# Optimization experiments

Measured on AMD Instinct MI355X. Metric: run time of the kernel, lower is better.

Reference implementation:

```python
import jax, jax.numpy as jnp
import numpy as np

N = 20000
E = 320000
DIM_IN, DIM_H, DIM_OUT, HEADS = 500, 32, 16, 8
NEG_SLOPE = 0.2


def _glorot(key, shape, fan_in, fan_out):
    s = jnp.sqrt(6.0 / (fan_in + fan_out))
    return jax.random.uniform(key, shape, jnp.float32, -s, s)


def setup_inputs() -> dict:
    key = jax.random.key(0)
    ks = jax.random.split(key, 16)
    x = jax.random.normal(ks[0], (N, DIM_IN), jnp.float32)
    edge_index = jax.random.randint(ks[1], (2, E), 0, N, jnp.int64)
    h1 = HEADS * DIM_H   # 256
    h2 = HEADS * DIM_OUT  # 128
    return {
        "x": x,
        "edge_index": edge_index,
        # layer 1: GATv2Conv(500, 32, heads=8), concat -> 256
        "W1l": _glorot(ks[2], (h1, DIM_IN), DIM_IN, h1),
        "b1l": jnp.zeros((h1,), jnp.float32),
        "W1r": _glorot(ks[3], (h1, DIM_IN), DIM_IN, h1),
        "b1r": jnp.zeros((h1,), jnp.float32),
        "att1": _glorot(ks[4], (HEADS, DIM_H), DIM_H, 1),
        "bias1": jnp.zeros((h1,), jnp.float32),
        # layer 2: GATv2Conv(256, 16, heads=8), concat -> 128
        "W2l": _glorot(ks[5], (h2, h1), h1, h2),
        "b2l": jnp.zeros((h2,), jnp.float32),
        "W2r": _glorot(ks[6], (h2, h1), h1, h2),
        "b2r": jnp.zeros((h2,), jnp.float32),
        "att2": _glorot(ks[7], (HEADS, DIM_OUT), DIM_OUT, 1),
        "bias2": jnp.zeros((h2,), jnp.float32),
    }


def _gatv2_layer(x, Wl, bl, Wr, br, att, bias, src, dst, heads, out_ch):
    n = x.shape[0]
    xl = (x @ Wl.T + bl).reshape(n, heads, out_ch)  # source transform
    xr = (x @ Wr.T + br).reshape(n, heads, out_ch)  # target transform
    e = xl[src] + xr[dst]                            # [E', H, C]
    e = jnp.where(e >= 0, e, NEG_SLOPE * e)          # LeakyReLU(0.2)
    logits = jnp.einsum('ehc,hc->eh', e, att)        # [E', H]
    # segment softmax over incoming edges of each dst node
    m = jax.ops.segment_max(logits, dst, num_segments=n)
    ex = jnp.exp(logits - m[dst])
    denom = jax.ops.segment_sum(ex, dst, num_segments=n)
    alpha = ex / denom[dst]                          # [E', H]
    out = jax.ops.segment_sum(xl[src] * alpha[:, :, None], dst, num_segments=n)
    return out.reshape(n, heads * out_ch) + bias


def reference(x, edge_index, W1l, b1l, W1r, b1r, att1, bias1,
              W2l, b2l, W2r, b2r, att2, bias2):
    n = x.shape[0]
    loop = jnp.arange(n, dtype=edge_index.dtype)
    src = jnp.concatenate([edge_index[0], loop])  # PyG add_self_loops=True
    dst = jnp.concatenate([edge_index[1], loop])
    h = _gatv2_layer(x, W1l, b1l, W1r, b1r, att1, bias1, src, dst, HEADS, DIM_H)
    h = jax.nn.elu(h)  # normalization='none' -> Identity; eval-mode dropout is identity
    h = _gatv2_layer(h, W2l, b2l, W2r, b2r, att2, bias2, src, dst, HEADS, DIM_OUT)
    return jax.nn.log_softmax(h, axis=1)
```

## Files before the change

### kernel.cpp

```cpp
#include <hip/hip_runtime.h>
#include <math.h>

#define DIN   500
#define H1    256
#define H2    128
#define NEG_SLOPE 0.2f

typedef __attribute__((ext_vector_type(8))) short short8;
typedef __attribute__((ext_vector_type(4))) float floatx4;

static __device__ __forceinline__ unsigned short f2bf(float f) {
    union { float f; unsigned int u; } x; x.f = f;
    unsigned int r = x.u + 0x7fffu + ((x.u >> 16) & 1u);
    return (unsigned short)(r >> 16);
}
static __device__ __forceinline__ float bitsf(unsigned int i) {
    union { unsigned int i; float f; } x; x.i = i;
    return x.f;
}
static __device__ __forceinline__ void cvt8(uint4 u, float* o) {
    o[0] = bitsf(u.x << 16); o[1] = bitsf(u.x & 0xffff0000u);
    o[2] = bitsf(u.y << 16); o[3] = bitsf(u.y & 0xffff0000u);
    o[4] = bitsf(u.z << 16); o[5] = bitsf(u.z & 0xffff0000u);
    o[6] = bitsf(u.w << 16); o[7] = bitsf(u.w & 0xffff0000u);
}


__global__ void count_deg(const int* __restrict__ dst, int E, int N,
                          int* __restrict__ counts) {
    int i = blockIdx.x * blockDim.x + threadIdx.x;
    int total = E + N;
    if (i < total) {
        int d = (i < E) ? dst[i] : (i - E);
        atomicAdd(&counts[d], 1);
    }
}

__global__ __launch_bounds__(1024) void block_scan(const int* __restrict__ counts,
                                                   int* __restrict__ excl,
                                                   int* __restrict__ bsum, int n) {
    __shared__ int s[1024];
    int tid = threadIdx.x;
    int i = blockIdx.x * 1024 + tid;
    int v = (i < n) ? counts[i] : 0;
    s[tid] = v;
    __syncthreads();
    #pragma unroll
    for (int off = 1; off < 1024; off <<= 1) {
        int t = (tid >= off) ? s[tid - off] : 0;
        __syncthreads();
        s[tid] += t;
        __syncthreads();
    }
    if (i < n) excl[i] = s[tid] - v;
    if (tid == 1023) bsum[blockIdx.x] = s[1023];
}

__global__ void scan_sums(int* __restrict__ bsum, int nb) {
    if (threadIdx.x == 0 && blockIdx.x == 0) {
        int run = 0;
        for (int i = 0; i < nb; ++i) { int t = bsum[i]; bsum[i] = run; run += t; }
    }
}

__global__ void add_base(const int* __restrict__ excl, const int* __restrict__ bsum,
                         int* __restrict__ offsets, int* __restrict__ cursor,
                         int n, int total) {
    int i = blockIdx.x * blockDim.x + threadIdx.x;
    if (i < n) {
        int o = excl[i] + bsum[i >> 10];
        offsets[i] = o;
        cursor[i]  = o;
    }
    if (i == 0) offsets[n] = total;
}

__global__ void scatter_edges(const int* __restrict__ src, const int* __restrict__ dst,
                              int E, int N, int* __restrict__ cursor,
                              int* __restrict__ esrc) {
    int i = blockIdx.x * blockDim.x + threadIdx.x;
    int total = E + N;
    if (i < total) {
        int d, s;
        if (i < E) { d = dst[i]; s = src[i]; }
        else       { d = i - E; s = i - E; }
        int pos = atomicAdd(&cursor[d], 1);
        esrc[pos] = s;
    }
}

static __device__ __forceinline__ void cast_body(const float* __restrict__ src,
                                                 unsigned short* __restrict__ dst,
                                                 int M, int K, int K2, long total, long base) {
    if (base >= total) return;
    int row = (int)(base / K2);
    int c   = (int)(base % K2);
    const float* srow = src + (size_t)row * K;
    unsigned short tmp[8];
    #pragma unroll
    for (int j = 0; j < 8; ++j) {
        int cc = c + j;
        float v = (row < M && cc < K) ? srow[cc] : 0.f;
        tmp[j] = f2bf(v);
    }
    *reinterpret_cast<int4*>(dst + base) = *reinterpret_cast<const int4*>(tmp);
}

__global__ void cast_pad(const float* __restrict__ src, unsigned short* __restrict__ dst,
                         int M, int K, int K2, long total) {
    long base = ((long)blockIdx.x * blockDim.x + threadIdx.x) * 8;
    cast_body(src, dst, M, K, K2, total, base);
}

__global__ void cast_wts(const float* __restrict__ W1l, const float* __restrict__ W1r,
                         const float* __restrict__ W2l, const float* __restrict__ W2r,
                         unsigned short* __restrict__ W1b, unsigned short* __restrict__ W2b,
                         int K1p) {
    long base = ((long)blockIdx.x * blockDim.x + threadIdx.x) * 8;
    switch (blockIdx.y) {
        case 0: cast_body(W1l, W1b,                      H1, DIN, K1p, (long)H1 * K1p, base); break;
        case 1: cast_body(W1r, W1b + (size_t)H1 * K1p,   H1, DIN, K1p, (long)H1 * K1p, base); break;
        case 2: cast_body(W2l, W2b,                      H2, H1,  H1,  (long)H2 * H1,  base); break;
        default: cast_body(W2r, W2b + (size_t)H2 * H1,   H2, H1,  H1,  (long)H2 * H1,  base); break;
    }
}

template<int MODE>
__global__ __launch_bounds__(256) void gemm_mfma(const unsigned short* __restrict__ A,
                                                 const unsigned short* __restrict__ W,
                                                 const float* __restrict__ b_lo,
                                                 const float* __restrict__ b_hi,
                                                 int halfN,
                                                 unsigned short* __restrict__ Cb,
                                                 float* __restrict__ Cf,
                                                 int M, int Nc, int K) {
    __shared__ unsigned short lA[128 * 64];
    __shared__ unsigned short lB[128 * 64];
    int tid  = threadIdx.x;
    int lane = tid & 63;
    int wid  = tid >> 6;
    int wr   = wid >> 1, wc = wid & 1;
    int bm = blockIdx.x * 128, bn = blockIdx.y * 128;

    floatx4 acc[4][4] = {};

    int st_r = (lane >> 3);
    int st_p = (lane & 7);

    for (int k0 = 0; k0 < K; k0 += 64) {
        #pragma unroll
        for (int i = 0; i < 4; ++i) {
            int r = i * 32 + wid * 8 + st_r;
            int s = st_p ^ (r & 7);
            const unsigned short* ga = A + (size_t)(bm + r) * K + k0 + s * 8;
            const unsigned short* gb = W + (size_t)(bn + r) * K + k0 + s * 8;
            __builtin_amdgcn_global_load_lds(
                (const __attribute__((address_space(1))) void*)ga,
                (__attribute__((address_space(3))) void*)((char*)lA + i * 4096 + wid * 1024),
                16, 0, 0);
            __builtin_amdgcn_global_load_lds(
                (const __attribute__((address_space(1))) void*)gb,
                (__attribute__((address_space(3))) void*)((char*)lB + i * 4096 + wid * 1024),
                16, 0, 0);
        }
        __syncthreads();

        #pragma unroll
        for (int kk = 0; kk < 2; ++kk) {
            int sbase = kk * 4 + (lane >> 4);
            short8 af[4], bf[4];
            #pragma unroll
            for (int ar = 0; ar < 4; ++ar) {
                int lr = wr * 64 + ar * 16 + (lane & 15);
                af[ar] = *reinterpret_cast<const short8*>(
                    (const char*)lA + lr * 128 + ((sbase ^ (lr & 7)) * 16));
            }
            #pragma unroll
            for (int bc = 0; bc < 4; ++bc) {
                int lc = wc * 64 + bc * 16 + (lane & 15);
                bf[bc] = *reinterpret_cast<const short8*>(
                    (const char*)lB + lc * 128 + ((sbase ^ (lc & 7)) * 16));
            }
            #pragma unroll
            for (int ar = 0; ar < 4; ++ar)
                #pragma unroll
                for (int bc = 0; bc < 4; ++bc)
                    acc[ar][bc] = __builtin_amdgcn_mfma_f32_16x16x32_bf16(
                        af[ar], bf[bc], acc[ar][bc], 0, 0, 0);
        }
        __syncthreads();
    }

    #pragma unroll
    for (int ar = 0; ar < 4; ++ar) {
        #pragma unroll
        for (int bc = 0; bc < 4; ++bc) {
            int col = bn + wc * 64 + bc * 16 + (lane & 15);
            float bv = (col < halfN) ? b_lo[col] : b_hi[col - halfN];
            #pragma unroll
            for (int r = 0; r < 4; ++r) {
                int row = bm + wr * 64 + ar * 16 + (lane >> 4) * 4 + r;
                if (row < M) {
                    float v = acc[ar][bc][r] + bv;
                    if (MODE == 1) {
                        Cb[(size_t)row * Nc + col] = f2bf(v);
                    } else {
                        if (col < halfN) Cb[(size_t)row * halfN + col] = f2bf(v);
                        else             Cf[(size_t)row * halfN + col - halfN] = v;
                    }
                }
            }
        }
    }
}

__global__ __launch_bounds__(256) void gat_edge1(const unsigned short* __restrict__ xlr,
                                                 const float* __restrict__ att,
                                                 const float* __restrict__ bias,
                                                 const int* __restrict__ offsets,
                                                 const int* __restrict__ esrc,
                                                 unsigned short* __restrict__ hb,
                                                 int N) {
    int node = blockIdx.x * 4 + (threadIdx.x >> 6);
    int lane = threadIdx.x & 63;
    int sub  = lane >> 4;
    int ln   = lane & 15;
    int c0   = ln * 16;
    if (node >= N) {
        if (sub == 0) {
            int4 z = {0, 0, 0, 0};
            int4* pp = reinterpret_cast<int4*>(&hb[(size_t)node * H1 + c0]);
            pp[0] = z; pp[1] = z;
        }
        return;
    }
    const unsigned short* xrrow = xlr + ((size_t)node << 9) + 256 + c0;
    float r_[16];
    cvt8(*reinterpret_cast<const uint4*>(xrrow),     r_);
    cvt8(*reinterpret_cast<const uint4*>(xrrow + 8), r_ + 8);
    float a_[16];
    #pragma unroll
    for (int j = 0; j < 4; ++j)
        *reinterpret_cast<float4*>(&a_[j * 4]) =
            *reinterpret_cast<const float4*>(&att[c0 + j * 4]);

    float d = 0.f;
    float ac[16];
    #pragma unroll
    for (int j = 0; j < 16; ++j) ac[j] = 0.f;

    int beg = offsets[node], end = offsets[node + 1];
    int k = beg + sub;
    bool v_c = (k < end);
    bool v_n = (k + 4 < end);
    int s_c = esrc[v_c ? k : beg];
    int s_n = esrc[v_n ? k + 4 : beg];
    const unsigned short* rc = xlr + ((size_t)s_c << 9) + c0;
    uint4 c0v = *reinterpret_cast<const uint4*>(rc);
    uint4 c1v = *reinterpret_cast<const uint4*>(rc + 8);

    while (v_c) {
        const unsigned short* rn = xlr + ((size_t)s_n << 9) + c0;
        uint4 n0v = *reinterpret_cast<const uint4*>(rn);
        uint4 n1v = *reinterpret_cast<const uint4*>(rn + 8);
        bool v_nn = (k + 8 < end);
        int s_nn = esrc[v_nn ? k + 8 : beg];

        float l_[16];
        cvt8(c0v, l_); cvt8(c1v, l_ + 8);
        float p0 = 0.f, p1 = 0.f;
        #pragma unroll
        for (int j = 0; j < 8; ++j) {
            float e0 = l_[j]     + r_[j];     e0 = fmaxf(e0, NEG_SLOPE * e0);
            float e1 = l_[j + 8] + r_[j + 8]; e1 = fmaxf(e1, NEG_SLOPE * e1);
            p0 = fmaf(e0, a_[j], p0);
            p1 = fmaf(e1, a_[j + 8], p1);
        }
        float p = p0 + p1;
        p += __shfl_xor(p, 1, 2);
        float w = __expf(p);
        d += w;
        #pragma unroll
        for (int j = 0; j < 16; ++j) ac[j] = fmaf(w, l_[j], ac[j]);

        c0v = n0v; c1v = n1v;
        s_c = s_n; s_n = s_nn;
        v_c = v_n; v_n = v_nn;
        k += 4;
    }

    #pragma unroll
    for (int off = 16; off <= 32; off <<= 1) {
        d += __shfl_xor(d, off, 64);
        #pragma unroll
        for (int j = 0; j < 16; ++j) ac[j] += __shfl_xor(ac[j], off, 64);
    }

    if (sub == 0) {
        float inv = 1.f / d;
        unsigned int ow[8];
        #pragma unroll
        for (int j = 0; j < 8; ++j) {
            float o0 = ac[2 * j]     * inv + bias[c0 + 2 * j];
            float o1 = ac[2 * j + 1] * inv + bias[c0 + 2 * j + 1];
            o0 = (o0 > 0.f) ? o0 : __expf(o0) - 1.f;
            o1 = (o1 > 0.f) ? o1 : __expf(o1) - 1.f;
            ow[j] = (unsigned int)f2bf(o0) | ((unsigned int)f2bf(o1) << 16);
        }
        uint4* pp = reinterpret_cast<uint4*>(&hb[(size_t)node * H1 + c0]);
        pp[0] = make_uint4(ow[0], ow[1], ow[2], ow[3]);
        pp[1] = make_uint4(ow[4], ow[5], ow[6], ow[7]);
    }
}

__global__ __launch_bounds__(256) void gat_edge2(const unsigned short* __restrict__ xl2b,
                                                 const float* __restrict__ xr2f,
                                                 const float* __restrict__ att,
                                                 const float* __restrict__ bias,
                                                 const int* __restrict__ offsets,
                                                 const int* __restrict__ esrc,
                                                 float* __restrict__ out,
                                                 int N) {
    int node = blockIdx.x * 4 + (threadIdx.x >> 6);
    if (node >= N) return;
    int lane = threadIdx.x & 63;
    int sub  = lane >> 4;
    int ln   = lane & 15;
    int c0   = ln * 8;

    float r_[8];
    *reinterpret_cast<float4*>(&r_[0]) =
        *reinterpret_cast<const float4*>(&xr2f[(size_t)node * H2 + c0]);
    *reinterpret_cast<float4*>(&r_[4]) =
        *reinterpret_cast<const float4*>(&xr2f[(size_t)node * H2 + c0 + 4]);
    float a_[8];
    *reinterpret_cast<float4*>(&a_[0]) = *reinterpret_cast<const float4*>(&att[c0]);
    *reinterpret_cast<float4*>(&a_[4]) = *reinterpret_cast<const float4*>(&att[c0 + 4]);

    float d = 0.f;
    float ac[8];
    #pragma unroll
    for (int j = 0; j < 8; ++j) ac[j] = 0.f;

    int beg = offsets[node], end = offsets[node + 1];
    int k = beg + sub;
    bool v_c = (k < end);
    bool v_n = (k + 4 < end);
    int s_c = esrc[v_c ? k : beg];
    int s_n = esrc[v_n ? k + 4 : beg];
    uint4 cv = *reinterpret_cast<const uint4*>(&xl2b[(size_t)s_c * H2 + c0]);

    while (v_c) {
        uint4 nv = *reinterpret_cast<const uint4*>(&xl2b[(size_t)s_n * H2 + c0]);
        bool v_nn = (k + 8 < end);
        int s_nn = esrc[v_nn ? k + 8 : beg];

        float l_[8];
        cvt8(cv, l_);
        float p0 = 0.f, p1 = 0.f;
        #pragma unroll
        for (int j = 0; j < 4; ++j) {
            float e0 = l_[j]     + r_[j];     e0 = fmaxf(e0, NEG_SLOPE * e0);
            float e1 = l_[j + 4] + r_[j + 4]; e1 = fmaxf(e1, NEG_SLOPE * e1);
            p0 = fmaf(e0, a_[j], p0);
            p1 = fmaf(e1, a_[j + 4], p1);
        }
        float p = p0 + p1;
        p += __shfl_xor(p, 1, 2);
        float w = __expf(p);
        d += w;
        #pragma unroll
        for (int j = 0; j < 8; ++j) ac[j] = fmaf(w, l_[j], ac[j]);

        cv = nv;
        s_c = s_n; s_n = s_nn;
        v_c = v_n; v_n = v_nn;
        k += 4;
    }

    #pragma unroll
    for (int off = 16; off <= 32; off <<= 1) {
        d += __shfl_xor(d, off, 64);
        #pragma unroll
        for (int j = 0; j < 8; ++j) ac[j] += __shfl_xor(ac[j], off, 64);
    }

    float inv = 1.f / d;
    float v[8];
    #pragma unroll
    for (int j = 0; j < 8; ++j) v[j] = ac[j] * inv + bias[c0 + j];
    float lm = v[0];
    #pragma unroll
    for (int j = 1; j < 8; ++j) lm = fmaxf(lm, v[j]);
    #pragma unroll
    for (int off = 1; off < 16; off <<= 1) lm = fmaxf(lm, __shfl_xor(lm, off, 16));
    float se = 0.f;
    #pragma unroll
    for (int j = 0; j < 8; ++j) se += __expf(v[j] - lm);
    #pragma unroll
    for (int off = 1; off < 16; off <<= 1) se += __shfl_xor(se, off, 16);
    float lz = lm + __logf(se);

    if (sub == 0) {
        float4 o0 = { v[0] - lz, v[1] - lz, v[2] - lz, v[3] - lz };
        float4 o1 = { v[4] - lz, v[5] - lz, v[6] - lz, v[7] - lz };
        float4* pp = reinterpret_cast<float4*>(&out[(size_t)node * H2 + c0]);
        pp[0] = o0; pp[1] = o1;
    }
}


extern "C" void kernel_launch(void* const* d_in, const int* in_sizes, int n_in,
                              void* d_out, int out_size, void* d_ws, size_t ws_size,
                              hipStream_t stream) {
    const float* x     = (const float*)d_in[0];
    const int*   ei    = (const int*)d_in[1];
    const float* W1l   = (const float*)d_in[2];
    const float* b1l   = (const float*)d_in[3];
    const float* W1r   = (const float*)d_in[4];
    const float* b1r   = (const float*)d_in[5];
    const float* att1  = (const float*)d_in[6];
    const float* bias1 = (const float*)d_in[7];
    const float* W2l   = (const float*)d_in[8];
    const float* b2l   = (const float*)d_in[9];
    const float* W2r   = (const float*)d_in[10];
    const float* b2r   = (const float*)d_in[11];
    const float* att2  = (const float*)d_in[12];
    const float* bias2 = (const float*)d_in[13];
    float* out = (float*)d_out;

    const int N  = in_sizes[0] / DIN;
    const int E  = in_sizes[1] / 2;
    const int EN = E + N;
    const int Mpad = ((N + 127) / 128) * 128;
    const int K1p  = 512;
    const int* srcIdx = ei;
    const int* dstIdx = ei + E;

    char* ws = (char*)d_ws;
    unsigned short* xb   = (unsigned short*)ws; ws += (size_t)Mpad * K1p * sizeof(short);
    unsigned short* W1b  = (unsigned short*)ws; ws += (size_t)(2 * H1) * K1p * sizeof(short);
    unsigned short* W2b  = (unsigned short*)ws; ws += (size_t)(2 * H2) * H1 * sizeof(short);
    unsigned short* xlr1 = (unsigned short*)ws; ws += (size_t)Mpad * (2 * H1) * sizeof(short);
    unsigned short* hb   = (unsigned short*)ws; ws += (size_t)Mpad * H1 * sizeof(short);
    unsigned short* xl2b = (unsigned short*)ws; ws += (size_t)Mpad * H2 * sizeof(short);
    float* xr2f = (float*)ws; ws += (size_t)Mpad * H2 * sizeof(float);
    int* counts  = (int*)ws;  ws += (size_t)N * sizeof(int);
    int* excl    = (int*)ws;  ws += (size_t)N * sizeof(int);
    int* bsum    = (int*)ws;  ws += 64 * sizeof(int);
    int* offsets = (int*)ws;  ws += (size_t)(N + 1) * sizeof(int);
    int* cursor  = (int*)ws;  ws += (size_t)N * sizeof(int);
    int* esrc    = (int*)ws;  ws += (size_t)EN * sizeof(int);

    const int nb = (N + 1023) / 1024;
    hipMemsetAsync(counts, 0, (size_t)N * sizeof(int), stream);
    count_deg<<<(EN + 255) / 256, 256, 0, stream>>>(dstIdx, E, N, counts);
    block_scan<<<nb, 1024, 0, stream>>>(counts, excl, bsum, N);
    scan_sums<<<1, 64, 0, stream>>>(bsum, nb);
    add_base<<<(N + 255) / 256, 256, 0, stream>>>(excl, bsum, offsets, cursor, N, EN);
    scatter_edges<<<(EN + 255) / 256, 256, 0, stream>>>(srcIdx, dstIdx, E, N, cursor, esrc);

    {
        long tot = (long)Mpad * K1p;
        cast_pad<<<(int)((tot / 8 + 255) / 256), 256, 0, stream>>>(x, xb, N, DIN, K1p, tot);
        long wmax = (long)H1 * K1p;
        dim3 gw((int)((wmax / 8 + 255) / 256), 4);
        cast_wts<<<gw, 256, 0, stream>>>(W1l, W1r, W2l, W2r, W1b, W2b, K1p);
    }

    dim3 g1(Mpad / 128, (2 * H1) / 128);
    gemm_mfma<1><<<g1, 256, 0, stream>>>(xb, W1b, b1l, b1r, H1, xlr1, nullptr, Mpad, 2 * H1, K1p);

    gat_edge1<<<Mpad / 4, 256, 0, stream>>>(xlr1, att1, bias1, offsets, esrc, hb, N);

    dim3 g2(Mpad / 128, (2 * H2) / 128);
    gemm_mfma<2><<<g2, 256, 0, stream>>>(hb, W2b, b2l, b2r, H2, xl2b, xr2f, N, 2 * H2, H1);

    gat_edge2<<<(N + 3) / 4, 256, 0, stream>>>(xl2b, xr2f, att2, bias2, offsets, esrc, out, N);
}
```

Baseline: 167.3 us.

## Merge preprocessing launches: fused cast/zero, single-pass scan, scatter inside GEMM1

Cuts the launch count. The memset and all bf16 casts go into one prep kernel, which sets degree counts to 1 so self-loops are counted without atomics. The three scan kernels become one, where the last-arriving block (found with an atomic ticket) computes block offsets and writes offsets and cursor. Edge scatter runs as extra blocks in the layer-1 GEMM grid. The goal is to remove launch gaps and small serial kernels, at the cost of a threadfence/ticket protocol and mixed-role blocks that may unbalance the GEMM.

```diff
diff --git a/kernel.cpp b/kernel.cpp
--- a/kernel.cpp
+++ b/kernel.cpp
@@ -25,23 +25,93 @@
     o[6] = bitsf(u.w << 16); o[7] = bitsf(u.w & 0xffff0000u);
 }
 
-
-__global__ void count_deg(const int* __restrict__ dst, int E, int N,
-                          int* __restrict__ counts) {
+template<int SHIFT>
+static __device__ __forceinline__ void cast_seg(const float* __restrict__ src,
+                                                unsigned short* __restrict__ dst,
+                                                int M, int K, long base, long total) {
+    if (base >= total) return;
+    int row = (int)(base >> SHIFT);
+    int c   = (int)(base & ((1 << SHIFT) - 1));
+    const float* srow = src + (size_t)row * K;
+    unsigned short tmp[8];
+    #pragma unroll
+    for (int j = 0; j < 8; ++j) {
+        int cc = c + j;
+        float v = (row < M && cc < K) ? srow[cc] : 0.f;
+        tmp[j] = f2bf(v);
+    }
+    *reinterpret_cast<int4*>(dst + base) = *reinterpret_cast<const int4*>(tmp);
+}
+
+__global__ __launch_bounds__(256) void prep(const float* __restrict__ x,
+                                            const float* __restrict__ W1l,
+                                            const float* __restrict__ W1r,
+                                            const float* __restrict__ W2l,
+                                            const float* __restrict__ W2r,
+                                            unsigned short* __restrict__ xb,
+                                            unsigned short* __restrict__ W1b,
+                                            unsigned short* __restrict__ W2b,
+                                            int* __restrict__ counts,
+                                            int N, int Mpad,
+                                            int ZB, int XB, int W1B, int W2B) {
+    int bid = blockIdx.x;
+    int tid = threadIdx.x;
+    if (bid < ZB) {
+        int i = bid * 256 + tid;
+        if (i < N) counts[i] = 1;
+        else if (i == N) counts[N] = 0;
+        return;
+    }
+    bid -= ZB;
+    if (bid < XB) {
+        long base = ((long)bid * 256 + tid) * 8;
+        cast_seg<9>(x, xb, N, DIN, base, (long)Mpad * 512);
+        return;
+    }
+    bid -= XB;
+    if (bid < W1B) {
+        long base = ((long)bid * 256 + tid) * 8;
+        cast_seg<9>(W1l, W1b, H1, DIN, base, (long)H1 * 512);
+        return;
+    }
+    bid -= W1B;
+    if (bid < W1B) {
+        long base = ((long)bid * 256 + tid) * 8;
+        cast_seg<9>(W1r, W1b + (size_t)H1 * 512, H1, DIN, base, (long)H1 * 512);
+        return;
+    }
+    bid -= W1B;
+    if (bid < W2B) {
+        long base = ((long)bid * 256 + tid) * 8;
+        cast_seg<8>(W2l, W2b, H2, H1, base, (long)H2 * H1);
+        return;
+    }
+    bid -= W2B;
+    {
+        long base = ((long)bid * 256 + tid) * 8;
+        cast_seg<8>(W2r, W2b + (size_t)H2 * H1, H2, H1, base, (long)H2 * H1);
+    }
+}
+
+
+__global__ void count_deg(const int* __restrict__ dst, int E, int* __restrict__ counts) {
     int i = blockIdx.x * blockDim.x + threadIdx.x;
-    int total = E + N;
-    if (i < total) {
-        int d = (i < E) ? dst[i] : (i - E);
-        atomicAdd(&counts[d], 1);
-    }
-}
-
-__global__ __launch_bounds__(1024) void block_scan(const int* __restrict__ counts,
-                                                   int* __restrict__ excl,
-                                                   int* __restrict__ bsum, int n) {
+    if (i < E) atomicAdd(&counts[dst[i]], 1);
+}
+
+__global__ __launch_bounds__(1024) void scan_all(const int* __restrict__ counts,
+                                                 int* __restrict__ excl,
+                                                 int* __restrict__ bsum,
+                                                 int* __restrict__ done,
+                                                 int* __restrict__ offsets,
+                                                 int* __restrict__ cursor,
+                                                 int n, int total_edges, int nb) {
     __shared__ int s[1024];
+    __shared__ int sb[32];
+    __shared__ int ticket;
     int tid = threadIdx.x;
-    int i = blockIdx.x * 1024 + tid;
+    int bid = blockIdx.x;
+    int i = bid * 1024 + tid;
     int v = (i < n) ? counts[i] : 0;
     s[tid] = v;
     __syncthreads();
@@ -53,94 +123,44 @@
         __syncthreads();
     }
     if (i < n) excl[i] = s[tid] - v;
-    if (tid == 1023) bsum[blockIdx.x] = s[1023];
-}
-
-__global__ void scan_sums(int* __restrict__ bsum, int nb) {
-    if (threadIdx.x == 0 && blockIdx.x == 0) {
-        int run = 0;
-        for (int i = 0; i < nb; ++i) { int t = bsum[i]; bsum[i] = run; run += t; }
-    }
-}
-
-__global__ void add_base(const int* __restrict__ excl, const int* __restrict__ bsum,
-                         int* __restrict__ offsets, int* __restrict__ cursor,
-                         int n, int total) {
-    int i = blockIdx.x * blockDim.x + threadIdx.x;
-    if (i < n) {
-        int o = excl[i] + bsum[i >> 10];
-        offsets[i] = o;
-        cursor[i]  = o;
-    }
-    if (i == 0) offsets[n] = total;
-}
-
-__global__ void scatter_edges(const int* __restrict__ src, const int* __restrict__ dst,
-                              int E, int N, int* __restrict__ cursor,
-                              int* __restrict__ esrc) {
-    int i = blockIdx.x * blockDim.x + threadIdx.x;
-    int total = E + N;
-    if (i < total) {
-        int d, s;
-        if (i < E) { d = dst[i]; s = src[i]; }
-        else       { d = i - E; s = i - E; }
-        int pos = atomicAdd(&cursor[d], 1);
-        esrc[pos] = s;
-    }
-}
-
-static __device__ __forceinline__ void cast_body(const float* __restrict__ src,
-                                                 unsigned short* __restrict__ dst,
-                                                 int M, int K, int K2, long total, long base) {
-    if (base >= total) return;
-    int row = (int)(base / K2);
-    int c   = (int)(base % K2);
-    const float* srow = src + (size_t)row * K;
-    unsigned short tmp[8];
-    #pragma unroll
-    for (int j = 0; j < 8; ++j) {
-        int cc = c + j;
-        float v = (row < M && cc < K) ? srow[cc] : 0.f;
-        tmp[j] = f2bf(v);
-    }
-    *reinterpret_cast<int4*>(dst + base) = *reinterpret_cast<const int4*>(tmp);
-}
-
-__global__ void cast_pad(const float* __restrict__ src, unsigned short* __restrict__ dst,
-                         int M, int K, int K2, long total) {
-    long base = ((long)blockIdx.x * blockDim.x + threadIdx.x) * 8;
-    cast_body(src, dst, M, K, K2, total, base);
-}
-
-__global__ void cast_wts(const float* __restrict__ W1l, const float* __restrict__ W1r,
-                         const float* __restrict__ W2l, const float* __restrict__ W2r,
-                         unsigned short* __restrict__ W1b, unsigned short* __restrict__ W2b,
-                         int K1p) {
-    long base = ((long)blockIdx.x * blockDim.x + threadIdx.x) * 8;
-    switch (blockIdx.y) {
-        case 0: cast_body(W1l, W1b,                      H1, DIN, K1p, (long)H1 * K1p, base); break;
-        case 1: cast_body(W1r, W1b + (size_t)H1 * K1p,   H1, DIN, K1p, (long)H1 * K1p, base); break;
-        case 2: cast_body(W2l, W2b,                      H2, H1,  H1,  (long)H2 * H1,  base); break;
-        default: cast_body(W2r, W2b + (size_t)H2 * H1,   H2, H1,  H1,  (long)H2 * H1,  base); break;
+    if (tid == 1023) bsum[bid] = s[1023];
+    __syncthreads();
+    if (tid == 0) {
+        __threadfence();
+        ticket = __hip_atomic_fetch_add(done, 1, __ATOMIC_ACQ_REL, __HIP_MEMORY_SCOPE_AGENT);
+    }
+    __syncthreads();
+    if (ticket == nb - 1) {
+        __threadfence();
+        if (tid == 0) {
+            int run = 0;
+            for (int j = 0; j < nb; ++j) { int t = bsum[j]; sb[j] = run; run += t; }
+        }
+        __syncthreads();
+        for (int j = tid; j < n; j += 1024) {
+            int o = excl[j] + sb[j >> 10];
+            offsets[j] = o;
+            cursor[j]  = o;
+        }
+        if (tid == 0) offsets[n] = total_edges;
     }
 }
 
 template<int MODE>
-__global__ __launch_bounds__(256) void gemm_mfma(const unsigned short* __restrict__ A,
+static __device__ __forceinline__ void gemm_body(unsigned short* lA, unsigned short* lB,
+                                                 const unsigned short* __restrict__ A,
                                                  const unsigned short* __restrict__ W,
                                                  const float* __restrict__ b_lo,
                                                  const float* __restrict__ b_hi,
                                                  int halfN,
                                                  unsigned short* __restrict__ Cb,
                                                  float* __restrict__ Cf,
-                                                 int M, int Nc, int K) {
-    __shared__ unsigned short lA[128 * 64];
-    __shared__ unsigned short lB[128 * 64];
+                                                 int M, int Nc, int K,
+                                                 int bm, int bn) {
     int tid  = threadIdx.x;
     int lane = tid & 63;
     int wid  = tid >> 6;
     int wr   = wid >> 1, wc = wid & 1;
-    int bm = blockIdx.x * 128, bn = blockIdx.y * 128;
 
     floatx4 acc[4][4] = {};
 
@@ -214,6 +234,50 @@
     }
 }
 
+__global__ __launch_bounds__(256) void gemm1_scatter(const unsigned short* __restrict__ A,
+                                                     const unsigned short* __restrict__ W,
+                                                     const float* __restrict__ b_lo,
+                                                     const float* __restrict__ b_hi,
+                                                     unsigned short* __restrict__ Cb,
+                                                     const int* __restrict__ src,
+                                                     const int* __restrict__ dst,
+                                                     int E, int N,
+                                                     int* __restrict__ cursor,
+                                                     int* __restrict__ esrc,
+                                                     int GB, int M, int Nc, int K) {
+    __shared__ unsigned short lA[128 * 64];
+    __shared__ unsigned short lB[128 * 64];
+    int bid = blockIdx.x;
+    if (bid < GB) {
+        gemm_body<1>(lA, lB, A, W, b_lo, b_hi, Nc >> 1, Cb, nullptr, M, Nc, K,
+                     (bid >> 2) * 128, (bid & 3) * 128);
+    } else {
+        int i = (bid - GB) * 256 + threadIdx.x;
+        int total = E + N;
+        if (i < total) {
+            int d, s;
+            if (i < E) { d = dst[i]; s = src[i]; }
+            else       { d = i - E; s = i - E; }
+            int pos = atomicAdd(&cursor[d], 1);
+            esrc[pos] = s;
+        }
+    }
+}
+
+__global__ __launch_bounds__(256) void gemm2_k(const unsigned short* __restrict__ A,
+                                               const unsigned short* __restrict__ W,
+                                               const float* __restrict__ b_lo,
+                                               const float* __restrict__ b_hi,
+                                               int halfN,
+                                               unsigned short* __restrict__ Cb,
+                                               float* __restrict__ Cf,
+                                               int M, int Nc, int K) {
+    __shared__ unsigned short lA[128 * 64];
+    __shared__ unsigned short lB[128 * 64];
+    gemm_body<2>(lA, lB, A, W, b_lo, b_hi, halfN, Cb, Cf, M, Nc, K,
+                 blockIdx.x * 128, blockIdx.y * 128);
+}
+
 __global__ __launch_bounds__(256) void gat_edge1(const unsigned short* __restrict__ xlr,
                                                  const float* __restrict__ att,
                                                  const float* __restrict__ bias,
@@ -445,36 +509,37 @@
     unsigned short* hb   = (unsigned short*)ws; ws += (size_t)Mpad * H1 * sizeof(short);
     unsigned short* xl2b = (unsigned short*)ws; ws += (size_t)Mpad * H2 * sizeof(short);
     float* xr2f = (float*)ws; ws += (size_t)Mpad * H2 * sizeof(float);
-    int* counts  = (int*)ws;  ws += (size_t)N * sizeof(int);
+    int* counts  = (int*)ws;  ws += (size_t)(N + 1) * sizeof(int);
     int* excl    = (int*)ws;  ws += (size_t)N * sizeof(int);
     int* bsum    = (int*)ws;  ws += 64 * sizeof(int);
     int* offsets = (int*)ws;  ws += (size_t)(N + 1) * sizeof(int);
     int* cursor  = (int*)ws;  ws += (size_t)N * sizeof(int);
     int* esrc    = (int*)ws;  ws += (size_t)EN * sizeof(int);
 
-    const int nb = (N + 1023) / 1024;
-    hipMemsetAsync(counts, 0, (size_t)N * sizeof(int), stream);
-    count_deg<<<(EN + 255) / 256, 256, 0, stream>>>(dstIdx, E, N, counts);
-    block_scan<<<nb, 1024, 0, stream>>>(counts, excl, bsum, N);
-    scan_sums<<<1, 64, 0, stream>>>(bsum, nb);
-    add_base<<<(N + 255) / 256, 256, 0, stream>>>(excl, bsum, offsets, cursor, N, EN);
-    scatter_edges<<<(EN + 255) / 256, 256, 0, stream>>>(srcIdx, dstIdx, E, N, cursor, esrc);
-
-    {
-        long tot = (long)Mpad * K1p;
-        cast_pad<<<(int)((tot / 8 + 255) / 256), 256, 0, stream>>>(x, xb, N, DIN, K1p, tot);
-        long wmax = (long)H1 * K1p;
-        dim3 gw((int)((wmax / 8 + 255) / 256), 4);
-        cast_wts<<<gw, 256, 0, stream>>>(W1l, W1r, W2l, W2r, W1b, W2b, K1p);
-    }
-
-    dim3 g1(Mpad / 128, (2 * H1) / 128);
-    gemm_mfma<1><<<g1, 256, 0, stream>>>(xb, W1b, b1l, b1r, H1, xlr1, nullptr, Mpad, 2 * H1, K1p);
+    const int ZB  = (N + 1 + 255) / 256;
+    const int XB  = (int)(((long)Mpad * K1p / 8 + 255) / 256);
+    const int W1B = (H1 * K1p / 8 + 255) / 256;
+    const int W2B = (H2 * H1 / 8 + 255) / 256;
+    const int nb  = (N + 1023) / 1024;
+
+    prep<<<ZB + XB + 2 * W1B + 2 * W2B, 256, 0, stream>>>(
+        x, W1l, W1r, W2l, W2r, xb, W1b, W2b, counts, N, Mpad, ZB, XB, W1B, W2B);
+
+    count_deg<<<(E + 255) / 256, 256, 0, stream>>>(dstIdx, E, counts);
+
+    scan_all<<<nb, 1024, 0, stream>>>(counts, excl, bsum, counts + N,
+                                      offsets, cursor, N, EN, nb);
+
+    const int GB = (Mpad / 128) * ((2 * H1) / 128);
+    const int SB = (EN + 255) / 256;
+    gemm1_scatter<<<GB + SB, 256, 0, stream>>>(xb, W1b, b1l, b1r, xlr1,
+                                               srcIdx, dstIdx, E, N, cursor, esrc,
+                                               GB, Mpad, 2 * H1, K1p);
 
     gat_edge1<<<Mpad / 4, 256, 0, stream>>>(xlr1, att1, bias1, offsets, esrc, hb, N);
 
-    dim3 g2(Mpad / 128, (2 * H2) / 128);
-    gemm_mfma<2><<<g2, 256, 0, stream>>>(hb, W2b, b2l, b2r, H2, xl2b, xr2f, N, 2 * H2, H1);
+    gemm2_k<<<dim3(Mpad / 128, (2 * H2) / 128), 256, 0, stream>>>(
+        hb, W2b, b2l, b2r, H2, xl2b, xr2f, N, 2 * H2, H1);
 
     gat_edge2<<<(N + 3) / 4, 256, 0, stream>>>(xl2b, xr2f, att2, bias2, offsets, esrc, out, N);
 }
```

New measurement: 152.8 us. 8.7% less time.
